# Kernel optimization log

Measured on AMD Instinct MI355X. Metric: run time of the kernel, lower is better.

The kernel has to match this reference:

```python
import jax, jax.numpy as jnp
import numpy as np

B, E, N, M = 2, 512, 4096, 4096

def setup_inputs() -> dict:
    key = jax.random.key(0)
    ks = jax.random.split(key, 8)
    s = 1.0 / np.sqrt(E)
    return {
        "src_embedding": jax.random.normal(ks[0], (B, E, N), jnp.float32),
        "tgt_embedding": jax.random.normal(ks[1], (B, E, M), jnp.float32),
        "src": jax.random.normal(ks[2], (B, 3, N), jnp.float32),
        "tgt": jax.random.normal(ks[3], (B, 3, M), jnp.float32),
        "Wq": jax.random.normal(ks[4], (E, E), jnp.float32) * s,
        "bq": jax.random.normal(ks[5], (E,), jnp.float32) * s,
        "Wk": jax.random.normal(ks[6], (E, E), jnp.float32) * s,
        "bk": jax.random.normal(ks[7], (E,), jnp.float32) * s,
    }

def reference(src_embedding, tgt_embedding, src, tgt, Wq, bq, Wk, bk):
    # query/key: [B, N, E] after transpose + Linear (y = x @ W^T + b)
    q = jnp.einsum('ben,fe->bnf', src_embedding, Wq) + bq
    k = jnp.einsum('bem,fe->bmf', tgt_embedding, Wk) + bk
    # pairwise_distance[b,n,m] = -||q_n||^2 + 2 q_n.k_m - ||k_m||^2 = -||q_n - k_m||^2
    inner = jnp.einsum('bne,bme->bnm', q, k)          # [B, N, M]
    qq = jnp.sum(q * q, axis=-1)                      # [B, N]
    kk = jnp.sum(k * k, axis=-1)                      # [B, M]
    pairwise = 2.0 * inner - qq[:, :, None] - kk[:, None, :]
    scores = jax.nn.softmax(pairwise, axis=2)         # softmax over keys (M)
    # src_corr = tgt @ scores^T : [B, 3, N]
    src_corr = jnp.einsum('bdm,bnm->bdn', tgt, scores)
    return (src, src_corr)
```

## Files before the change

### kernel.cpp

```cpp
#include <hip/hip_runtime.h>


typedef _Float16 f16;
typedef __attribute__((ext_vector_type(8))) _Float16 f16x8;
typedef __attribute__((ext_vector_type(4))) float f32x4;

constexpr int B_ = 2, E_ = 512, N_ = 4096, M_ = 4096;
constexpr int MCH = 8;
constexpr float WSCALE = 64.0f;

__device__ __forceinline__ f32x4 mfma16(f16x8 a, f16x8 b, f32x4 c) {
  return __builtin_amdgcn_mfma_f32_16x16x32_f16(a, b, c, 0, 0, 0);
}
__device__ __forceinline__ void gll16(const void* g, void* l) {
  __builtin_amdgcn_global_load_lds(
      (const __attribute__((address_space(1))) unsigned int*)g,
      (__attribute__((address_space(3))) unsigned int*)l, 16, 0, 0);
}
__device__ __forceinline__ void waitv8() { asm volatile("s_waitcnt vmcnt(8)" ::: "memory"); }
__device__ __forceinline__ void waitv0() { asm volatile("s_waitcnt vmcnt(0)" ::: "memory"); }


__global__ void k_split_w(const float* __restrict__ Wq, const float* __restrict__ Wk,
                          f16* __restrict__ WqH, f16* __restrict__ WqL,
                          f16* __restrict__ WkH, f16* __restrict__ WkL) {
  int i = blockIdx.x * 256 + threadIdx.x;
  float a = Wq[i] * WSCALE;
  f16 ah = (f16)a; WqH[i] = ah; WqL[i] = (f16)(a - (float)ah);
  float b = Wk[i] * WSCALE;
  f16 bh = (f16)b; WkH[i] = bh; WkL[i] = (f16)(b - (float)bh);
}

__global__ void k_tsplit(const float* __restrict__ Xq, const float* __restrict__ Xk,
                         f16* __restrict__ XqH, f16* __restrict__ XqL,
                         f16* __restrict__ XkH, f16* __restrict__ XkL) {
  __shared__ float tile[64][65];
  const int b = blockIdx.z >> 1, which = blockIdx.z & 1;
  const float* X = (which ? Xk : Xq) + (size_t)b * E_ * N_;
  f16* H = (which ? XkH : XqH) + (size_t)b * N_ * E_;
  f16* L = (which ? XkL : XqL) + (size_t)b * N_ * E_;
  const int e0 = blockIdx.x * 64, n0 = blockIdx.y * 64;
  const int x = threadIdx.x, y = threadIdx.y;
#pragma unroll
  for (int j = 0; j < 16; ++j) {
    int e = y * 16 + j;
    tile[e][x] = X[(size_t)(e0 + e) * N_ + n0 + x];
  }
  __syncthreads();
#pragma unroll
  for (int j = 0; j < 16; ++j) {
    int nl = y * 16 + j;
    float v = tile[x][nl];
    f16 h = (f16)v;
    H[(size_t)(n0 + nl) * E_ + e0 + x] = h;
    L[(size_t)(n0 + nl) * E_ + e0 + x] = (f16)(v - (float)h);
  }
}

__global__ __launch_bounds__(256, 2) void k_proj(
    const f16* __restrict__ XqH, const f16* __restrict__ XqL,
    const f16* __restrict__ XkH, const f16* __restrict__ XkL,
    const f16* __restrict__ WqH, const f16* __restrict__ WqL,
    const f16* __restrict__ WkH, const f16* __restrict__ WkL,
    const float* __restrict__ bq, const float* __restrict__ bk,
    f16* __restrict__ QH, f16* __restrict__ QL,
    f16* __restrict__ KH, f16* __restrict__ KL) {
  __shared__ char lds[65536];
  const int b = blockIdx.z >> 1, kind = blockIdx.z & 1;
  const f16* AH = (kind ? XkH : XqH) + (size_t)b * N_ * E_;
  const f16* AL = (kind ? XkL : XqL) + (size_t)b * N_ * E_;
  const f16* BH = kind ? WkH : WqH;
  const f16* BL = kind ? WkL : WqL;
  const float* bias = kind ? bk : bq;
  f16* OH = (kind ? KH : QH) + (size_t)b * N_ * E_;
  f16* OL = (kind ? KL : QL) + (size_t)b * N_ * E_;
  const int n0 = blockIdx.x * 128, f0 = blockIdx.y * 128;
  const int l = threadIdx.x & 63, w = threadIdx.x >> 6;
  const int wr = (w >> 1) * 64, wc = (w & 1) * 64;
  const int r15 = l & 15;

  const int q = (l & 7) ^ (l >> 3);
  const size_t soff = (size_t)(w * 8 + (l >> 3)) * E_ + (q & 3) * 8;
  const f16* sA = (q < 4 ? AH : AL) + (size_t)n0 * E_ + soff;
  const f16* sB = (q < 4 ? BH : BL) + (size_t)f0 * E_ + soff;

  auto STAGE = [&](int k) {
    char* dA = lds + ((k & 1) << 14) + w * 1024;
    char* dB = lds + 32768 + ((k & 1) << 14) + w * 1024;
    const f16* pa = sA + k * 32;
    const f16* pb = sB + k * 32;
#pragma unroll
    for (int c = 0; c < 4; ++c) {
      gll16(pa + (size_t)c * 32 * E_, dA + c * 4096);
      gll16(pb + (size_t)c * 32 * E_, dB + c * 4096);
    }
  };

  const int pH16 = ((l >> 4) ^ (l & 7)) * 16;
  const int aoffH = (wr + r15) * 128 + pH16;
  const int boffH = (wc + r15) * 128 + pH16;

  f32x4 acc[4][4] = {};
  STAGE(0);
#pragma unroll 2
  for (int k = 0; k < 16; ++k) {
    if (k < 15) { STAGE(k + 1); waitv8(); } else { waitv0(); }
    __builtin_amdgcn_sched_barrier(0);
    __builtin_amdgcn_s_barrier();
    const char* cA = lds + ((k & 1) << 14);
    const char* cB = lds + 32768 + ((k & 1) << 14);
    f16x8 ah[4], al[4], bh[4], bl[4];
#pragma unroll
    for (int i = 0; i < 4; ++i) {
      ah[i] = *(const f16x8*)(cA + aoffH + i * 2048);
      al[i] = *(const f16x8*)(cA + (aoffH ^ 64) + i * 2048);
      bh[i] = *(const f16x8*)(cB + boffH + i * 2048);
      bl[i] = *(const f16x8*)(cB + (boffH ^ 64) + i * 2048);
    }
    __builtin_amdgcn_s_setprio(1);
#pragma unroll
    for (int i = 0; i < 4; ++i)
#pragma unroll
      for (int j = 0; j < 4; ++j) {
        acc[i][j] = mfma16(ah[i], bh[j], acc[i][j]);
        acc[i][j] = mfma16(ah[i], bl[j], acc[i][j]);
        acc[i][j] = mfma16(al[i], bh[j], acc[i][j]);
      }
    __builtin_amdgcn_s_setprio(0);
    __builtin_amdgcn_s_barrier();
  }

  const int rowg = (l >> 4) * 4;
#pragma unroll
  for (int j = 0; j < 4; ++j) {
    int f = f0 + wc + j * 16 + r15;
    float bv = bias[f];
#pragma unroll
    for (int i = 0; i < 4; ++i) {
#pragma unroll
      for (int r = 0; r < 4; ++r) {
        int n = n0 + wr + i * 16 + rowg + r;
        float qv = acc[i][j][r] * (1.0f / WSCALE) + bv;
        f16 h = (f16)qv;
        OH[(size_t)n * E_ + f] = h;
        OL[(size_t)n * E_ + f] = (f16)(qv - (float)h);
      }
    }
  }
}

__global__ void k_kk(const f16* __restrict__ KH, const f16* __restrict__ KL,
                     float* __restrict__ kk) {
  int row = blockIdx.x * 4 + (threadIdx.x >> 6);
  int lane = threadIdx.x & 63;
  f16x8 h8 = *(const f16x8*)(KH + (size_t)row * E_ + lane * 8);
  f16x8 l8 = *(const f16x8*)(KL + (size_t)row * E_ + lane * 8);
  float s = 0.f;
#pragma unroll
  for (int i = 0; i < 8; ++i) {
    float v = (float)h8[i] + (float)l8[i];
    s += v * v;
  }
#pragma unroll
  for (int o = 32; o; o >>= 1) s += __shfl_xor(s, o);
  if (lane == 0) kk[row] = s;
}

__global__ __launch_bounds__(256, 2) void k_flash(
    const f16* __restrict__ QH, const f16* __restrict__ QL,
    const f16* __restrict__ KH, const f16* __restrict__ KL,
    const float* __restrict__ kk, const float* __restrict__ tgt,
    float* __restrict__ part) {
  __shared__ char lds[73728];
  float* kks = (float*)(lds + 65536);
  float* tgs = (float*)(lds + 67584);
  const int b = blockIdx.z;
  const int n0 = blockIdx.x * 128;
  const int mc = blockIdx.y, m0c = mc * 512;
  const int tid = threadIdx.x, l = tid & 63, w = tid >> 6;
  const int r15 = l & 15;

  for (int i = tid; i < 512; i += 256) kks[i] = kk[(size_t)b * M_ + m0c + i];
  for (int i = tid; i < 1536; i += 256) {
    int d = i >> 9, m = i & 511;
    tgs[i] = tgt[((size_t)b * 3 + d) * M_ + m0c + m];
  }

  const f16* AH = QH + ((size_t)b * N_ + n0) * E_;
  const f16* AL = QL + ((size_t)b * N_ + n0) * E_;
  const f16* BHb = KH + ((size_t)b * M_ + m0c) * E_;
  const f16* BLb = KL + ((size_t)b * M_ + m0c) * E_;

  const int q = (l & 7) ^ (l >> 3);
  const size_t soff = (size_t)(w * 8 + (l >> 3)) * E_ + (q & 3) * 8;
  const f16* sA = (q < 4 ? AH : AL) + soff;
  const f16* sB = (q < 4 ? BHb : BLb) + soff;

  auto STAGE = [&](int s) {
    int mt_ = s >> 4, k_ = s & 15;
    char* dA = lds + ((s & 1) << 14) + w * 1024;
    char* dB = lds + 32768 + ((s & 1) << 14) + w * 1024;
    const f16* pa = sA + k_ * 32;
    const f16* pb = sB + (size_t)mt_ * 128 * E_ + k_ * 32;
#pragma unroll
    for (int c = 0; c < 4; ++c) {
      gll16(pa + (size_t)c * 32 * E_, dA + c * 4096);
      gll16(pb + (size_t)c * 32 * E_, dB + c * 4096);
    }
  };

  const int pH16 = ((l >> 4) ^ (l & 7)) * 16;
  const int aoffH = (w * 32 + r15) * 128 + pH16;
  const int boffH = r15 * 128 + pH16;

  float mrun[8], psum[8], pp0[8], pp1[8], pp2[8];
#pragma unroll
  for (int x = 0; x < 8; ++x) {
    mrun[x] = -3.0e38f; psum[x] = 0.f; pp0[x] = 0.f; pp1[x] = 0.f; pp2[x] = 0.f;
  }

  STAGE(0);
  for (int mt = 0; mt < 4; ++mt) {
    f32x4 acc[2][8] = {};
#pragma unroll 2
    for (int k = 0; k < 16; ++k) {
      const int s = mt * 16 + k;
      if (s < 63) { STAGE(s + 1); waitv8(); } else { waitv0(); }
      __builtin_amdgcn_sched_barrier(0);
      __builtin_amdgcn_s_barrier();
      const char* cA = lds + ((s & 1) << 14);
      const char* cB = lds + 32768 + ((s & 1) << 14);
      f16x8 ah0 = *(const f16x8*)(cA + aoffH);
      f16x8 ah1 = *(const f16x8*)(cA + aoffH + 2048);
      f16x8 al0 = *(const f16x8*)(cA + (aoffH ^ 64));
      f16x8 al1 = *(const f16x8*)(cA + (aoffH ^ 64) + 2048);
      __builtin_amdgcn_s_setprio(1);
#pragma unroll
      for (int j = 0; j < 8; ++j) {
        f16x8 bh = *(const f16x8*)(cB + boffH + j * 2048);
        f16x8 bl = *(const f16x8*)(cB + (boffH ^ 64) + j * 2048);
        acc[0][j] = mfma16(ah0, bh, acc[0][j]);
        acc[1][j] = mfma16(ah1, bh, acc[1][j]);
        acc[0][j] = mfma16(ah0, bl, acc[0][j]);
        acc[1][j] = mfma16(ah1, bl, acc[1][j]);
        acc[0][j] = mfma16(al0, bh, acc[0][j]);
        acc[1][j] = mfma16(al1, bh, acc[1][j]);
      }
      __builtin_amdgcn_s_setprio(0);
      __builtin_amdgcn_s_barrier();
    }

    float kv[8], tv0[8], tv1[8], tv2[8];
#pragma unroll
    for (int j = 0; j < 8; ++j) {
      int ml = mt * 128 + j * 16 + r15;
      kv[j] = kks[ml];
      tv0[j] = tgs[ml];
      tv1[j] = tgs[512 + ml];
      tv2[j] = tgs[1024 + ml];
    }
#pragma unroll
    for (int i = 0; i < 2; ++i) {
#pragma unroll
      for (int r = 0; r < 4; ++r) {
        const int x = i * 4 + r;
        float s[8];
        float rmax = -3.0e38f;
#pragma unroll
        for (int j = 0; j < 8; ++j) {
          s[j] = 2.0f * acc[i][j][r] - kv[j];
          rmax = fmaxf(rmax, s[j]);
        }
        rmax = fmaxf(rmax, __shfl_xor(rmax, 1));
        rmax = fmaxf(rmax, __shfl_xor(rmax, 2));
        rmax = fmaxf(rmax, __shfl_xor(rmax, 4));
        rmax = fmaxf(rmax, __shfl_xor(rmax, 8));
        float nm = fmaxf(mrun[x], rmax);
        float sc = __expf(mrun[x] - nm);
        mrun[x] = nm;
        psum[x] *= sc; pp0[x] *= sc; pp1[x] *= sc; pp2[x] *= sc;
#pragma unroll
        for (int j = 0; j < 8; ++j) {
          float e = __expf(s[j] - nm);
          psum[x] += e;
          pp0[x] += e * tv0[j];
          pp1[x] += e * tv1[j];
          pp2[x] += e * tv2[j];
        }
      }
    }
  }

#pragma unroll
  for (int x = 0; x < 8; ++x) {
#pragma unroll
    for (int o = 1; o <= 8; o <<= 1) {
      psum[x] += __shfl_xor(psum[x], o);
      pp0[x] += __shfl_xor(pp0[x], o);
      pp1[x] += __shfl_xor(pp1[x], o);
      pp2[x] += __shfl_xor(pp2[x], o);
    }
  }
  if (r15 == 0) {
    const int hi = l >> 4;
#pragma unroll
    for (int x = 0; x < 8; ++x) {
      int i = x >> 2, r = x & 3;
      int n = n0 + w * 32 + i * 16 + hi * 4 + r;
      size_t pb = ((size_t)(b * N_ + n) * MCH + mc) * 5;
      part[pb + 0] = mrun[x];
      part[pb + 1] = psum[x];
      part[pb + 2] = pp0[x];
      part[pb + 3] = pp1[x];
      part[pb + 4] = pp2[x];
    }
  }
}

__global__ void k_comb(const float* __restrict__ part, float* __restrict__ out) {
  int idx = blockIdx.x * 256 + threadIdx.x;
  int b = idx >> 12, n = idx & (N_ - 1);
  const float* p = part + (size_t)idx * MCH * 5;
  float M = -3.0e38f;
#pragma unroll
  for (int c = 0; c < MCH; ++c) M = fmaxf(M, p[c * 5]);
  float S = 0.f, P0 = 0.f, P1 = 0.f, P2 = 0.f;
#pragma unroll
  for (int c = 0; c < MCH; ++c) {
    float e = __expf(p[c * 5] - M);
    S += p[c * 5 + 1] * e;
    P0 += p[c * 5 + 2] * e;
    P1 += p[c * 5 + 3] * e;
    P2 += p[c * 5 + 4] * e;
  }
  float inv = 1.0f / S;
  float* oc = out + (size_t)B_ * 3 * N_;
  oc[((size_t)b * 3 + 0) * N_ + n] = P0 * inv;
  oc[((size_t)b * 3 + 1) * N_ + n] = P1 * inv;
  oc[((size_t)b * 3 + 2) * N_ + n] = P2 * inv;
}

__global__ void k_copy(const float* __restrict__ src, float* __restrict__ out) {
  int i = blockIdx.x * 256 + threadIdx.x;
  out[i] = src[i];
}

extern "C" void kernel_launch(void* const* d_in, const int* in_sizes, int n_in,
                              void* d_out, int out_size, void* d_ws, size_t ws_size,
                              hipStream_t stream) {
  const float* src_emb = (const float*)d_in[0];
  const float* tgt_emb = (const float*)d_in[1];
  const float* src     = (const float*)d_in[2];
  const float* tgt     = (const float*)d_in[3];
  const float* Wq      = (const float*)d_in[4];
  const float* bq      = (const float*)d_in[5];
  const float* Wk      = (const float*)d_in[6];
  const float* bk      = (const float*)d_in[7];
  float* out = (float*)d_out;

  constexpr size_t SZX = (size_t)B_ * N_ * E_;
  constexpr size_t OFFW = 4 * SZX * sizeof(f16);
  constexpr size_t OFFQ = OFFW + 4 * (size_t)E_ * E_ * sizeof(f16);
  constexpr size_t OFFK2 = OFFQ + 4 * SZX * sizeof(f16);
  constexpr size_t OFFP = OFFK2 + (size_t)B_ * M_ * sizeof(float);
  constexpr size_t NEED = OFFP + (size_t)B_ * N_ * MCH * 5 * sizeof(float);
  if (ws_size < NEED) return;

  char* ws = (char*)d_ws;
  f16* XqH = (f16*)(ws);
  f16* XqL = XqH + SZX;
  f16* XkH = XqL + SZX;
  f16* XkL = XkH + SZX;
  f16* WqH = (f16*)(ws + OFFW);
  f16* WqL = WqH + (size_t)E_ * E_;
  f16* WkH = WqL + (size_t)E_ * E_;
  f16* WkL = WkH + (size_t)E_ * E_;
  f16* QH = (f16*)(ws + OFFQ);
  f16* QL = QH + SZX;
  f16* KH = QL + SZX;
  f16* KL = KH + SZX;
  float* kk = (float*)(ws + OFFK2);
  float* part = (float*)(ws + OFFP);

  k_split_w<<<dim3(E_ * E_ / 256), 256, 0, stream>>>(Wq, Wk, WqH, WqL, WkH, WkL);
  k_tsplit<<<dim3(E_ / 64, N_ / 64, B_ * 2), dim3(64, 4), 0, stream>>>(
      src_emb, tgt_emb, XqH, XqL, XkH, XkL);
  k_proj<<<dim3(N_ / 128, E_ / 128, B_ * 2), 256, 0, stream>>>(
      XqH, XqL, XkH, XkL, WqH, WqL, WkH, WkL, bq, bk, QH, QL, KH, KL);
  k_kk<<<dim3(B_ * M_ / 4), 256, 0, stream>>>(KH, KL, kk);
  k_flash<<<dim3(N_ / 128, MCH, B_), 256, 0, stream>>>(QH, QL, KH, KL, kk, tgt, part);
  k_comb<<<dim3(B_ * N_ / 256), 256, 0, stream>>>(part, out);
  k_copy<<<dim3(B_ * 3 * N_ / 256), 256, 0, stream>>>(src, out);
}
```

Measured before the change: 237.9 us.

## Overlap softmax with next tile MFMA, fuse kk into projection and merge output kernels

The flash kernel now double-buffers the score accumulators and runs the online-softmax update for the previous key tile in two bursts inside the next tile's MFMA k-loop, so exp/reduction work interleaves with matrix work. The softmax is vectorised over four rows, and kk/tgt are staged in a swizzled LDS layout so each lane reads them with vector loads. The key-norm computation is folded into the projection epilogue via shuffles and atomicAdd, which needs a memset and removes the k_kk kernel. The combine and copy kernels are merged into one launch. Together these cut launches and expose more overlap, at the cost of higher register pressure from the second accumulator set and the atomics.

```diff
diff --git a/kernel.cpp b/kernel.cpp
--- a/kernel.cpp
+++ b/kernel.cpp
@@ -19,6 +19,18 @@
 }
 __device__ __forceinline__ void waitv8() { asm volatile("s_waitcnt vmcnt(8)" ::: "memory"); }
 __device__ __forceinline__ void waitv0() { asm volatile("s_waitcnt vmcnt(0)" ::: "memory"); }
+__device__ __forceinline__ f32x4 vmax4(f32x4 a, f32x4 b) {
+  f32x4 r;
+  r[0] = fmaxf(a[0], b[0]); r[1] = fmaxf(a[1], b[1]);
+  r[2] = fmaxf(a[2], b[2]); r[3] = fmaxf(a[3], b[3]);
+  return r;
+}
+__device__ __forceinline__ f32x4 vexp4(f32x4 a) {
+  f32x4 r;
+  r[0] = __expf(a[0]); r[1] = __expf(a[1]);
+  r[2] = __expf(a[2]); r[3] = __expf(a[3]);
+  return r;
+}
 
 
 __global__ void k_split_w(const float* __restrict__ Wq, const float* __restrict__ Wk,
@@ -64,7 +76,8 @@
     const f16* __restrict__ WkH, const f16* __restrict__ WkL,
     const float* __restrict__ bq, const float* __restrict__ bk,
     f16* __restrict__ QH, f16* __restrict__ QL,
-    f16* __restrict__ KH, f16* __restrict__ KL) {
+    f16* __restrict__ KH, f16* __restrict__ KL,
+    float* __restrict__ kkout) {
   __shared__ char lds[65536];
   const int b = blockIdx.z >> 1, kind = blockIdx.z & 1;
   const f16* AH = (kind ? XkH : XqH) + (size_t)b * N_ * E_;
@@ -131,6 +144,11 @@
   }
 
   const int rowg = (l >> 4) * 4;
+  float kkp[4][4];
+#pragma unroll
+  for (int i = 0; i < 4; ++i)
+#pragma unroll
+    for (int r = 0; r < 4; ++r) kkp[i][r] = 0.f;
 #pragma unroll
   for (int j = 0; j < 4; ++j) {
     int f = f0 + wc + j * 16 + r15;
@@ -144,26 +162,24 @@
         f16 h = (f16)qv;
         OH[(size_t)n * E_ + f] = h;
         OL[(size_t)n * E_ + f] = (f16)(qv - (float)h);
+        kkp[i][r] += qv * qv;
       }
     }
   }
-}
-
-__global__ void k_kk(const f16* __restrict__ KH, const f16* __restrict__ KL,
-                     float* __restrict__ kk) {
-  int row = blockIdx.x * 4 + (threadIdx.x >> 6);
-  int lane = threadIdx.x & 63;
-  f16x8 h8 = *(const f16x8*)(KH + (size_t)row * E_ + lane * 8);
-  f16x8 l8 = *(const f16x8*)(KL + (size_t)row * E_ + lane * 8);
-  float s = 0.f;
-#pragma unroll
-  for (int i = 0; i < 8; ++i) {
-    float v = (float)h8[i] + (float)l8[i];
-    s += v * v;
-  }
-#pragma unroll
-  for (int o = 32; o; o >>= 1) s += __shfl_xor(s, o);
-  if (lane == 0) kk[row] = s;
+  if (kind) {
+#pragma unroll
+    for (int i = 0; i < 4; ++i)
+#pragma unroll
+      for (int r = 0; r < 4; ++r) {
+        float v = kkp[i][r];
+        v += __shfl_xor(v, 1); v += __shfl_xor(v, 2);
+        v += __shfl_xor(v, 4); v += __shfl_xor(v, 8);
+        if (r15 == 0) {
+          int n = n0 + wr + i * 16 + rowg + r;
+          atomicAdd(&kkout[(size_t)b * M_ + n], v);
+        }
+      }
+  }
 }
 
 __global__ __launch_bounds__(256, 2) void k_flash(
@@ -172,19 +188,22 @@
     const float* __restrict__ kk, const float* __restrict__ tgt,
     float* __restrict__ part) {
   __shared__ char lds[73728];
-  float* kks = (float*)(lds + 65536);
-  float* tgs = (float*)(lds + 67584);
+  float* ksw = (float*)(lds + 65536);
   const int b = blockIdx.z;
   const int n0 = blockIdx.x * 128;
   const int mc = blockIdx.y, m0c = mc * 512;
   const int tid = threadIdx.x, l = tid & 63, w = tid >> 6;
   const int r15 = l & 15;
 
-  for (int i = tid; i < 512; i += 256) kks[i] = kk[(size_t)b * M_ + m0c + i];
-  for (int i = tid; i < 1536; i += 256) {
-    int d = i >> 9, m = i & 511;
-    tgs[i] = tgt[((size_t)b * 3 + d) * M_ + m0c + m];
-  }
+  for (int idx = tid; idx < 512; idx += 256) {
+    int mt = idx >> 7, rem = idx & 127, j = rem >> 4, rr = rem & 15;
+    int dst = (mt * 16 + rr) * 8 + j;
+    ksw[dst]        = kk[(size_t)b * M_ + m0c + idx];
+    ksw[512 + dst]  = tgt[((size_t)b * 3 + 0) * M_ + m0c + idx];
+    ksw[1024 + dst] = tgt[((size_t)b * 3 + 1) * M_ + m0c + idx];
+    ksw[1536 + dst] = tgt[((size_t)b * 3 + 2) * M_ + m0c + idx];
+  }
+  __syncthreads();
 
   const f16* AH = QH + ((size_t)b * N_ + n0) * E_;
   const f16* AL = QL + ((size_t)b * N_ + n0) * E_;
@@ -213,15 +232,58 @@
   const int aoffH = (w * 32 + r15) * 128 + pH16;
   const int boffH = r15 * 128 + pH16;
 
-  float mrun[8], psum[8], pp0[8], pp1[8], pp2[8];
-#pragma unroll
-  for (int x = 0; x < 8; ++x) {
-    mrun[x] = -3.0e38f; psum[x] = 0.f; pp0[x] = 0.f; pp1[x] = 0.f; pp2[x] = 0.f;
-  }
-
-  STAGE(0);
-  for (int mt = 0; mt < 4; ++mt) {
-    f32x4 acc[2][8] = {};
+  f32x4 mrunA = {-3.0e38f, -3.0e38f, -3.0e38f, -3.0e38f};
+  f32x4 mrunB = {-3.0e38f, -3.0e38f, -3.0e38f, -3.0e38f};
+  f32x4 psumA = {}, p0A = {}, p1A = {}, p2A = {};
+  f32x4 psumB = {}, p0B = {}, p1B = {}, p2B = {};
+
+  auto BURST = [&](const f32x4 (&aP)[2][8], int i01, int pmt,
+                   f32x4& mrun, f32x4& psum, f32x4& p0, f32x4& p1, f32x4& p2)
+      __attribute__((always_inline)) {
+    const float* bp = ksw + (pmt * 16 + r15) * 8;
+    f32x4 kvL = *(const f32x4*)(bp);
+    f32x4 kvH = *(const f32x4*)(bp + 4);
+    f32x4 t0L = *(const f32x4*)(bp + 512),  t0H = *(const f32x4*)(bp + 516);
+    f32x4 t1L = *(const f32x4*)(bp + 1024), t1H = *(const f32x4*)(bp + 1028);
+    f32x4 t2L = *(const f32x4*)(bp + 1536), t2H = *(const f32x4*)(bp + 1540);
+    float kv[8]  = {kvL[0], kvL[1], kvL[2], kvL[3], kvH[0], kvH[1], kvH[2], kvH[3]};
+    float tv0[8] = {t0L[0], t0L[1], t0L[2], t0L[3], t0H[0], t0H[1], t0H[2], t0H[3]};
+    float tv1[8] = {t1L[0], t1L[1], t1L[2], t1L[3], t1H[0], t1H[1], t1H[2], t1H[3]};
+    float tv2[8] = {t2L[0], t2L[1], t2L[2], t2L[3], t2H[0], t2H[1], t2H[2], t2H[3]};
+    f32x4 sv[8];
+    f32x4 mx = {-3.0e38f, -3.0e38f, -3.0e38f, -3.0e38f};
+#pragma unroll
+    for (int j = 0; j < 8; ++j) {
+      sv[j] = 2.0f * aP[i01][j] - kv[j];
+      mx = vmax4(mx, sv[j]);
+    }
+#pragma unroll
+    for (int e = 0; e < 4; ++e) {
+      float v = mx[e];
+      v = fmaxf(v, __shfl_xor(v, 1)); v = fmaxf(v, __shfl_xor(v, 2));
+      v = fmaxf(v, __shfl_xor(v, 4)); v = fmaxf(v, __shfl_xor(v, 8));
+      mx[e] = v;
+    }
+    f32x4 nm = vmax4(mrun, mx);
+    f32x4 sc = vexp4(mrun - nm);
+    mrun = nm;
+    psum *= sc; p0 *= sc; p1 *= sc; p2 *= sc;
+#pragma unroll
+    for (int j = 0; j < 8; ++j) {
+      f32x4 e4 = vexp4(sv[j] - nm);
+      psum += e4;
+      p0 += e4 * tv0[j];
+      p1 += e4 * tv1[j];
+      p2 += e4 * tv2[j];
+    }
+  };
+
+  auto TILE = [&](int mt, f32x4 (&acc)[2][8], const f32x4 (&aP)[2][8], bool doSM)
+      __attribute__((always_inline)) {
+#pragma unroll
+    for (int i = 0; i < 2; ++i)
+#pragma unroll
+      for (int j = 0; j < 8; ++j) acc[i][j] = f32x4{0.f, 0.f, 0.f, 0.f};
 #pragma unroll 2
     for (int k = 0; k < 16; ++k) {
       const int s = mt * 16 + k;
@@ -248,101 +310,77 @@
       }
       __builtin_amdgcn_s_setprio(0);
       __builtin_amdgcn_s_barrier();
-    }
-
-    float kv[8], tv0[8], tv1[8], tv2[8];
-#pragma unroll
-    for (int j = 0; j < 8; ++j) {
-      int ml = mt * 128 + j * 16 + r15;
-      kv[j] = kks[ml];
-      tv0[j] = tgs[ml];
-      tv1[j] = tgs[512 + ml];
-      tv2[j] = tgs[1024 + ml];
-    }
-#pragma unroll
-    for (int i = 0; i < 2; ++i) {
-#pragma unroll
-      for (int r = 0; r < 4; ++r) {
-        const int x = i * 4 + r;
-        float s[8];
-        float rmax = -3.0e38f;
-#pragma unroll
-        for (int j = 0; j < 8; ++j) {
-          s[j] = 2.0f * acc[i][j][r] - kv[j];
-          rmax = fmaxf(rmax, s[j]);
-        }
-        rmax = fmaxf(rmax, __shfl_xor(rmax, 1));
-        rmax = fmaxf(rmax, __shfl_xor(rmax, 2));
-        rmax = fmaxf(rmax, __shfl_xor(rmax, 4));
-        rmax = fmaxf(rmax, __shfl_xor(rmax, 8));
-        float nm = fmaxf(mrun[x], rmax);
-        float sc = __expf(mrun[x] - nm);
-        mrun[x] = nm;
-        psum[x] *= sc; pp0[x] *= sc; pp1[x] *= sc; pp2[x] *= sc;
-#pragma unroll
-        for (int j = 0; j < 8; ++j) {
-          float e = __expf(s[j] - nm);
-          psum[x] += e;
-          pp0[x] += e * tv0[j];
-          pp1[x] += e * tv1[j];
-          pp2[x] += e * tv2[j];
-        }
-      }
-    }
-  }
-
-#pragma unroll
-  for (int x = 0; x < 8; ++x) {
-#pragma unroll
-    for (int o = 1; o <= 8; o <<= 1) {
-      psum[x] += __shfl_xor(psum[x], o);
-      pp0[x] += __shfl_xor(pp0[x], o);
-      pp1[x] += __shfl_xor(pp1[x], o);
-      pp2[x] += __shfl_xor(pp2[x], o);
-    }
-  }
+      if (doSM && k == 7)  BURST(aP, 0, mt - 1, mrunA, psumA, p0A, p1A, p2A);
+      if (doSM && k == 15) BURST(aP, 1, mt - 1, mrunB, psumB, p0B, p1B, p2B);
+    }
+  };
+
+  f32x4 accE[2][8], accO[2][8];
+  STAGE(0);
+  TILE(0, accE, accO, false);
+  TILE(1, accO, accE, true);
+  TILE(2, accE, accO, true);
+  TILE(3, accO, accE, true);
+  BURST(accO, 0, 3, mrunA, psumA, p0A, p1A, p2A);
+  BURST(accO, 1, 3, mrunB, psumB, p0B, p1B, p2B);
+
+  auto RED = [&](f32x4& v) __attribute__((always_inline)) {
+#pragma unroll
+    for (int e = 0; e < 4; ++e) {
+      float x = v[e];
+      x += __shfl_xor(x, 1); x += __shfl_xor(x, 2);
+      x += __shfl_xor(x, 4); x += __shfl_xor(x, 8);
+      v[e] = x;
+    }
+  };
+  RED(psumA); RED(p0A); RED(p1A); RED(p2A);
+  RED(psumB); RED(p0B); RED(p1B); RED(p2B);
+
   if (r15 == 0) {
     const int hi = l >> 4;
 #pragma unroll
-    for (int x = 0; x < 8; ++x) {
-      int i = x >> 2, r = x & 3;
-      int n = n0 + w * 32 + i * 16 + hi * 4 + r;
-      size_t pb = ((size_t)(b * N_ + n) * MCH + mc) * 5;
-      part[pb + 0] = mrun[x];
-      part[pb + 1] = psum[x];
-      part[pb + 2] = pp0[x];
-      part[pb + 3] = pp1[x];
-      part[pb + 4] = pp2[x];
-    }
-  }
-}
-
-__global__ void k_comb(const float* __restrict__ part, float* __restrict__ out) {
-  int idx = blockIdx.x * 256 + threadIdx.x;
-  int b = idx >> 12, n = idx & (N_ - 1);
-  const float* p = part + (size_t)idx * MCH * 5;
-  float M = -3.0e38f;
-#pragma unroll
-  for (int c = 0; c < MCH; ++c) M = fmaxf(M, p[c * 5]);
-  float S = 0.f, P0 = 0.f, P1 = 0.f, P2 = 0.f;
-#pragma unroll
-  for (int c = 0; c < MCH; ++c) {
-    float e = __expf(p[c * 5] - M);
-    S += p[c * 5 + 1] * e;
-    P0 += p[c * 5 + 2] * e;
-    P1 += p[c * 5 + 3] * e;
-    P2 += p[c * 5 + 4] * e;
-  }
-  float inv = 1.0f / S;
-  float* oc = out + (size_t)B_ * 3 * N_;
-  oc[((size_t)b * 3 + 0) * N_ + n] = P0 * inv;
-  oc[((size_t)b * 3 + 1) * N_ + n] = P1 * inv;
-  oc[((size_t)b * 3 + 2) * N_ + n] = P2 * inv;
-}
-
-__global__ void k_copy(const float* __restrict__ src, float* __restrict__ out) {
-  int i = blockIdx.x * 256 + threadIdx.x;
-  out[i] = src[i];
+    for (int i = 0; i < 2; ++i)
+#pragma unroll
+      for (int r = 0; r < 4; ++r) {
+        int n = n0 + w * 32 + i * 16 + hi * 4 + r;
+        size_t pb = ((size_t)(b * N_ + n) * MCH + mc) * 5;
+        part[pb + 0] = i ? mrunB[r] : mrunA[r];
+        part[pb + 1] = i ? psumB[r] : psumA[r];
+        part[pb + 2] = i ? p0B[r] : p0A[r];
+        part[pb + 3] = i ? p1B[r] : p1A[r];
+        part[pb + 4] = i ? p2B[r] : p2A[r];
+      }
+  }
+}
+
+__global__ void k_out(const float* __restrict__ part, const float* __restrict__ src,
+                      float* __restrict__ out) {
+  int gid = blockIdx.x * 256 + threadIdx.x;
+  if (blockIdx.x < B_ * N_ / 256) {
+    int idx = gid;
+    int b = idx >> 12, n = idx & (N_ - 1);
+    const float* p = part + (size_t)idx * MCH * 5;
+    float M = -3.0e38f;
+#pragma unroll
+    for (int c = 0; c < MCH; ++c) M = fmaxf(M, p[c * 5]);
+    float S = 0.f, P0 = 0.f, P1 = 0.f, P2 = 0.f;
+#pragma unroll
+    for (int c = 0; c < MCH; ++c) {
+      float e = __expf(p[c * 5] - M);
+      S += p[c * 5 + 1] * e;
+      P0 += p[c * 5 + 2] * e;
+      P1 += p[c * 5 + 3] * e;
+      P2 += p[c * 5 + 4] * e;
+    }
+    float inv = 1.0f / S;
+    float* oc = out + (size_t)B_ * 3 * N_;
+    oc[((size_t)b * 3 + 0) * N_ + n] = P0 * inv;
+    oc[((size_t)b * 3 + 1) * N_ + n] = P1 * inv;
+    oc[((size_t)b * 3 + 2) * N_ + n] = P2 * inv;
+  } else {
+    int i = gid - B_ * N_;
+    out[i] = src[i];
+  }
 }
 
 extern "C" void kernel_launch(void* const* d_in, const int* in_sizes, int n_in,
@@ -385,10 +423,9 @@
   k_split_w<<<dim3(E_ * E_ / 256), 256, 0, stream>>>(Wq, Wk, WqH, WqL, WkH, WkL);
   k_tsplit<<<dim3(E_ / 64, N_ / 64, B_ * 2), dim3(64, 4), 0, stream>>>(
       src_emb, tgt_emb, XqH, XqL, XkH, XkL);
+  hipMemsetAsync(kk, 0, (size_t)B_ * M_ * sizeof(float), stream);
   k_proj<<<dim3(N_ / 128, E_ / 128, B_ * 2), 256, 0, stream>>>(
-      XqH, XqL, XkH, XkL, WqH, WqL, WkH, WkL, bq, bk, QH, QL, KH, KL);
-  k_kk<<<dim3(B_ * M_ / 4), 256, 0, stream>>>(KH, KL, kk);
+      XqH, XqL, XkH, XkL, WqH, WqL, WkH, WkL, bq, bk, QH, QL, KH, KL, kk);
   k_flash<<<dim3(N_ / 128, MCH, B_), 256, 0, stream>>>(QH, QL, KH, KL, kk, tgt, part);
-  k_comb<<<dim3(B_ * N_ / 256), 256, 0, stream>>>(part, out);
-  k_copy<<<dim3(B_ * 3 * N_ / 256), 256, 0, stream>>>(src, out);
-}
+  k_out<<<dim3(B_ * N_ / 256 + B_ * 3 * N_ / 256), 256, 0, stream>>>(part, src, out);
+}
```

After: 238.2 us. Within noise of the previous version (+0.1%).
